# Kernel tuning notes

Measured on AMD Instinct MI355X. Metric: run time of the kernel, lower is better.

The kernel has to match this reference:

```python
import jax, jax.numpy as jnp
import numpy as np

LAYERS, HIDDEN, FFN, HEADS = 4, 128, 256, 4
HEAD_D = HIDDEN // HEADS          # 32
V_HEAD = 2 * HEAD_D               # 64 (double_v_dim)
V_DIM = 2 * HIDDEN                # 256
SCALE_BASE = 512
EPS = 1e-5
GAMMAS = (1.0 - np.exp(np.linspace(np.log(1.0 / 32), np.log(1.0 / 512), HEADS))).astype(np.float32)


def _xpos(x, downscale):
    # x: (..., L, d) -- xpos rotary embedding with per-position decay scale
    L, d = x.shape[-2], x.shape[-1]
    half = d // 2
    base_scale = (jnp.arange(half, dtype=jnp.float32) + 0.4 * d) / (1.4 * d)   # (half,)
    power = jnp.arange(L, dtype=jnp.float32)[:, None] / SCALE_BASE
    sc = base_scale[None, :] ** power                                          # (L, half)
    inv_freq = 1.0 / (10000.0 ** (jnp.arange(half, dtype=jnp.float32) / half))
    ang = jnp.arange(L, dtype=jnp.float32)[:, None] * inv_freq[None, :]        # (L, half)
    sin, cos = jnp.sin(ang), jnp.cos(ang)
    if downscale:
        sc = 1.0 / sc
    sin_d = jnp.repeat(sin * sc, 2, axis=-1)   # duplicate_interleave -> (L, d)
    cos_d = jnp.repeat(cos * sc, 2, axis=-1)
    x1, x2 = x[..., ::2], x[..., 1::2]
    rot = jnp.stack((-x2, x1), axis=-1).reshape(x.shape)  # rotate_every_two
    return x * cos_d + rot * sin_d


def _layer_norm(x, w, b):
    mu = x.mean(-1, keepdims=True)
    var = x.var(-1, keepdims=True)
    return (x - mu) / jnp.sqrt(var + EPS) * w + b


def _msr(X, wq, wk, wv, wg, wo, gn_w, gn_b):
    # MultiScaleRetention, parallel form. X: (B, L, HIDDEN)
    B, L, _ = X.shape
    Q = _xpos(jnp.einsum('blh,nhd->bnld', X, wq), False)   # (B, heads, L, 32)
    K = _xpos(jnp.einsum('blh,nhd->bnld', X, wk), True)
    V = jnp.einsum('blh,nhv->bnlv', X, wv)                 # (B, heads, L, 64)
    n = jnp.arange(L)
    diff = n[:, None] - n[None, :]
    gam = jnp.asarray(GAMMAS)[:, None, None]
    D = jnp.where(diff >= 0, gam ** jnp.maximum(diff, 0).astype(jnp.float32), 0.0)  # (heads, L, L)
    scores = jnp.einsum('bnld,bnmd->bnlm', Q, K) * D[None]
    Y = jnp.einsum('bnlm,bnmv->bnlv', scores, V)
    Y = Y.transpose(0, 2, 1, 3).reshape(B, L, V_DIM)       # concat heads on feature dim
    # GroupNorm(heads, V_DIM) over the channel axis
    Yg = Y.reshape(B, L, HEADS, V_HEAD)
    mu = Yg.mean(-1, keepdims=True)
    var = Yg.var(-1, keepdims=True)
    Yn = ((Yg - mu) / jnp.sqrt(var + EPS)).reshape(B, L, V_DIM) * gn_w + gn_b
    G = X @ wg
    return (G * jax.nn.sigmoid(G) * Yn) @ wo               # swish gate, output proj


def _forward(x, rem_w1, rem_b1, rem_w2, rem_b2, rem_w3, rem_b3,
             wq, wk, wv, wg, wo, gn_w, gn_b,
             ln1_w, ln1_b, ln2_w, ln2_b,
             ffn_w1, ffn_b1, ffn_w2, ffn_b2,
             dec_w1, dec_b1, dec_w2, dec_b2):
    gelu = lambda t: jax.nn.gelu(t, approximate=False)
    # REM: 5 -> 32 -> 64 -> 128, GELU after each linear
    X = gelu(gelu(gelu(x @ rem_w1 + rem_b1) @ rem_w2 + rem_b2) @ rem_w3 + rem_b3)
    # RetNet: pre-LN retention + pre-LN FFN blocks with residuals
    for i in range(LAYERS):
        Y = _msr(_layer_norm(X, ln1_w[i], ln1_b[i]), wq[i], wk[i], wv[i],
                 wg[i], wo[i], gn_w[i], gn_b[i]) + X
        Z = _layer_norm(Y, ln2_w[i], ln2_b[i])
        X = gelu(Z @ ffn_w1[i] + ffn_b1[i]) @ ffn_w2[i] + ffn_b2[i] + Y
    # Decoder: 128 -> 64 -> 20, softmax over classes
    logits = gelu(X @ dec_w1 + dec_b1) @ dec_w2 + dec_b2
    return jax.nn.softmax(logits, axis=-1)


def setup_inputs() -> dict:
    key = jax.random.key(0)
    ks = jax.random.split(key, 16)
    rn = lambda k, shape, s=0.02: jax.random.normal(k, shape, dtype=jnp.float32) * s
    B, L = 64, 512
    return {
        'x': jax.random.normal(ks[0], (B, L, 5), dtype=jnp.float32),
        'rem_w1': rn(ks[1], (5, 32)), 'rem_b1': jnp.zeros((32,), jnp.float32),
        'rem_w2': rn(ks[2], (32, 64)), 'rem_b2': jnp.zeros((64,), jnp.float32),
        'rem_w3': rn(ks[3], (64, HIDDEN)), 'rem_b3': jnp.zeros((HIDDEN,), jnp.float32),
        'wq': rn(ks[4], (LAYERS, HEADS, HIDDEN, HEAD_D), 1.0 / HIDDEN),
        'wk': rn(ks[5], (LAYERS, HEADS, HIDDEN, HEAD_D), 1.0 / HIDDEN),
        'wv': rn(ks[6], (LAYERS, HEADS, HIDDEN, V_HEAD), 1.0 / HIDDEN),
        'wg': rn(ks[7], (LAYERS, HIDDEN, V_DIM), 1.0 / HIDDEN),
        'wo': rn(ks[8], (LAYERS, V_DIM, HIDDEN), 1.0 / HIDDEN),
        'gn_w': jnp.ones((LAYERS, V_DIM), jnp.float32),
        'gn_b': jnp.zeros((LAYERS, V_DIM), jnp.float32),
        'ln1_w': jnp.ones((LAYERS, HIDDEN), jnp.float32),
        'ln1_b': jnp.zeros((LAYERS, HIDDEN), jnp.float32),
        'ln2_w': jnp.ones((LAYERS, HIDDEN), jnp.float32),
        'ln2_b': jnp.zeros((LAYERS, HIDDEN), jnp.float32),
        'ffn_w1': rn(ks[9], (LAYERS, HIDDEN, FFN)),
        'ffn_b1': jnp.zeros((LAYERS, FFN), jnp.float32),
        'ffn_w2': rn(ks[10], (LAYERS, FFN, HIDDEN)),
        'ffn_b2': jnp.zeros((LAYERS, HIDDEN), jnp.float32),
        'dec_w1': rn(ks[11], (HIDDEN, 64)), 'dec_b1': jnp.zeros((64,), jnp.float32),
        'dec_w2': rn(ks[12], (64, 20)), 'dec_b2': jnp.zeros((20,), jnp.float32),
    }


def reference(x, rem_w1, rem_b1, rem_w2, rem_b2, rem_w3, rem_b3,
              wq, wk, wv, wg, wo, gn_w, gn_b,
              ln1_w, ln1_b, ln2_w, ln2_b,
              ffn_w1, ffn_b1, ffn_w2, ffn_b2,
              dec_w1, dec_b1, dec_w2, dec_b2):
    return _forward(x, rem_w1, rem_b1, rem_w2, rem_b2, rem_w3, rem_b3,
                    wq, wk, wv, wg, wo, gn_w, gn_b,
                    ln1_w, ln1_b, ln2_w, ln2_b,
                    ffn_w1, ffn_b1, ffn_w2, ffn_b2,
                    dec_w1, dec_b1, dec_w2, dec_b2)
```

## Files before the change

### kernel.cpp

```cpp
#include <hip/hip_runtime.h>
#include <math.h>
#include <cmath>

#define SEQ   512
#define NBATCH 64
#define BT    32768
#define HID   128
#define NHEAD 4
#define HD    32
#define VHD   64
#define VDIM  256
#define FFND  256

typedef __attribute__((ext_vector_type(8))) short bf16x8;
typedef __attribute__((ext_vector_type(4))) float f32x4;
typedef unsigned short u16;

__device__ __forceinline__ float gelu_f(float x){ return 0.5f*x*(1.f+erff(x*0.70710678118f)); }

__device__ __forceinline__ u16 f2bf(float f){
  union{float f; unsigned u;} v; v.f = f;
  unsigned r = v.u + 0x7FFF + ((v.u>>16)&1);
  return (u16)(r>>16);
}
__device__ __forceinline__ float bf2f(u16 u){
  union{unsigned u; float f;} v; v.u = ((unsigned)u)<<16; return v.f;
}

__device__ __forceinline__ void gload16(const void* g, void* l){
  __builtin_amdgcn_global_load_lds(
      (const __attribute__((address_space(1))) unsigned*)g,
      (__attribute__((address_space(3))) unsigned*)l, 16, 0, 0);
}

#define STAGE_TILE_N(dst, base, strideU16, colOffU16, wid_, srow_, phys16l_, NIT) \
  do{                                                                           \
    _Pragma("unroll")                                                           \
    for(int it_=0; it_<NIT; it_++){                                             \
      int blk_ = (wid_)*NIT + it_;                                              \
      int row_ = blk_*4 + (srow_);                                              \
      int log16_ = (phys16l_) ^ (row_&15);                                      \
      gload16((base) + (size_t)row_*(strideU16) + (colOffU16) + log16_*8,       \
              &(dst)[blk_*512]);                                                \
    }                                                                           \
  }while(0)

#define STAGE_TILE(dst, base, strideU16, colOffU16, wid_, srow_, phys16l_) \
  STAGE_TILE_N(dst, base, strideU16, colOffU16, wid_, srow_, phys16l_, 8)

__global__ __launch_bounds__(256) void wconv_kernel(
    const float* __restrict__ wq, const float* __restrict__ wk,
    const float* __restrict__ wv, const float* __restrict__ wg,
    const float* __restrict__ wo, const float* __restrict__ f1,
    const float* __restrict__ f2, const float* __restrict__ dw1,
    const float* __restrict__ w2e, const float* __restrict__ w3e,
    u16* __restrict__ Wt)
{
  int idx = blockIdx.x*256 + threadIdx.x;
  if(idx >= 786432){
    int q = idx - 786432;
    if(q < 8192){ int col=q>>7, h=q&127; Wt[idx]=f2bf(dw1[h*64+col]); }
    else if(q < 10240){ int p=q-8192; int row=p>>5, col=p&31; Wt[idx]=f2bf(w2e[col*64+row]); }
    else { int p=q-10240; int row=p>>6, col=p&63; Wt[idx]=f2bf(w3e[col*128+row]); }
    return;
  }
  int layer = idx / 196608;
  int r = idx - layer*196608;
  u16* W = Wt + (size_t)layer*196608;
  const float* wq_l = wq + (size_t)layer*16384;
  const float* wk_l = wk + (size_t)layer*16384;
  const float* wv_l = wv + (size_t)layer*32768;
  const float* wg_l = wg + (size_t)layer*32768;
  const float* wo_l = wo + (size_t)layer*32768;
  const float* f1_l = f1 + (size_t)layer*32768;
  const float* f2_l = f2 + (size_t)layer*32768;
  float v;
  if(r < 98304){
    int col = r>>7, h = r&127;
    if(col<128){ int n=col>>5, d=col&31; v = wq_l[(n*128+h)*32+d]; }
    else if(col<256){ int c=col-128, n=c>>5, d=c&31; v = wk_l[(n*128+h)*32+d]; }
    else if(col<512){ int c=col-256, n=c>>6, j=c&63; v = wv_l[(n*128+h)*64+j]; }
    else { int p=col-512; v = wg_l[h*256+p]; }
    W[r] = f2bf(v);
  } else if(r < 131072){
    int q = r-98304; int col=q>>8, k=q&255;
    W[r] = f2bf(wo_l[k*128+col]);
  } else if(r < 163840){
    int q = r-131072; int col=q>>7, h=q&127;
    W[r] = f2bf(f1_l[h*256+col]);
  } else {
    int q = r-163840; int col=q>>8, k=q&255;
    W[r] = f2bf(f2_l[k*128+col]);
  }
}

__global__ __launch_bounds__(256) void embed_kernel(
    const float* __restrict__ x,
    const float* __restrict__ w1, const float* __restrict__ b1,
    const float* __restrict__ b2, const float* __restrict__ b3,
    const u16* __restrict__ W23t,
    const float* __restrict__ lnw, const float* __restrict__ lnb,
    float* __restrict__ X, u16* __restrict__ xn)
{
  __shared__ float sx[64][6];
  __shared__ float sw1[160], sb1[32], sb2[64], sb3[128];
  __shared__ u16 big[18944];
  int t=threadIdx.x, lane=t&63, wid=t>>6, mrow=lane&15, quad=lane>>4, r0=wid*16;
  int tok0=blockIdx.x*64;

  for(int i=t;i<320;i+=256) sx[i/5][i%5]=x[(size_t)tok0*5+i];
  for(int i=t;i<160;i+=256) sw1[i]=w1[i];
  if(t<32) sb1[t]=b1[t];
  if(t<64) sb2[t]=b2[t];
  if(t<128) sb3[t]=b3[t];
  for(int c=t;c<256;c+=256){ int row=c>>2, c8=(c&3)*8;
    *(uint4*)&big[2560+row*40+c8]=*(const uint4*)&W23t[row*32+c8]; }
  for(int c=t;c<1024;c+=256){ int row=c>>3, c8=(c&7)*8;
    *(uint4*)&big[9728+row*72+c8]=*(const uint4*)&W23t[2048+row*64+c8]; }
  __syncthreads();

  for(int task=t; task<2048; task+=256){
    int tok=task>>5, j=task&31;
    float a=sb1[j];
    #pragma unroll
    for(int i=0;i<5;i++) a+=sx[tok][i]*sw1[i*32+j];
    big[tok*40+j]=f2bf(gelu_f(a));
  }
  __syncthreads();

  f32x4 h2[4];
  #pragma unroll
  for(int cc=0;cc<4;cc++) h2[cc]=(f32x4){0.f,0.f,0.f,0.f};
  {
    bf16x8 a=*(const bf16x8*)&big[(r0+mrow)*40+quad*8];
    #pragma unroll
    for(int cc=0;cc<4;cc++){
      bf16x8 b=*(const bf16x8*)&big[2560+(cc*16+mrow)*40+quad*8];
      h2[cc]=__builtin_amdgcn_mfma_f32_16x16x32_bf16(a,b,h2[cc],0,0,0);
    }
  }
  #pragma unroll
  for(int cc=0;cc<4;cc++){
    float bs=sb2[cc*16+mrow];
    #pragma unroll
    for(int reg=0;reg<4;reg++)
      big[5120+(r0+quad*4+reg)*72+cc*16+mrow]=f2bf(gelu_f(h2[cc][reg]+bs));
  }
  __syncthreads();

  f32x4 xac[8];
  #pragma unroll
  for(int cc=0;cc<8;cc++) xac[cc]=(f32x4){0.f,0.f,0.f,0.f};
  #pragma unroll
  for(int ks=0;ks<2;ks++){
    bf16x8 a=*(const bf16x8*)&big[5120+(r0+mrow)*72+ks*32+quad*8];
    #pragma unroll
    for(int cc=0;cc<8;cc++){
      bf16x8 b=*(const bf16x8*)&big[9728+(cc*16+mrow)*72+ks*32+quad*8];
      xac[cc]=__builtin_amdgcn_mfma_f32_16x16x32_bf16(a,b,xac[cc],0,0,0);
    }
  }
  __syncthreads();

  #pragma unroll
  for(int reg=0;reg<4;reg++){
    int rowl=r0+quad*4+reg, rowg=tok0+rowl;
    float xv[8], s=0.f, sq=0.f;
    #pragma unroll
    for(int cc=0;cc<8;cc++){
      float v=gelu_f(xac[cc][reg]+sb3[cc*16+mrow]);
      xv[cc]=v; s+=v; sq+=v*v;
    }
    #pragma unroll
    for(int m=1;m<16;m<<=1){ s+=__shfl_xor(s,m); sq+=__shfl_xor(sq,m); }
    float mu=s*(1.f/128.f);
    float var=sq*(1.f/128.f)-mu*mu;
    float rstd=rsqrtf(var+1e-5f);
    #pragma unroll
    for(int cc=0;cc<8;cc++){
      int col=cc*16+mrow;
      X[(size_t)rowg*128+col]=xv[cc];
      big[rowl*136+col]=f2bf((xv[cc]-mu)*rstd*lnw[col]+lnb[col]);
    }
  }
  __syncthreads();
  for(int th=t; th<1024; th+=256){
    int row=th>>4, seg=th&15;
    *(uint4*)&xn[(size_t)(tok0+row)*128+seg*8]=*(const uint4*)&big[row*136+seg*8];
  }
}

__device__ __forceinline__ void qkvg_epilogue(
    int nc, f32x4 acc[2][4], u16* stg,
    int t, int mrow, int quad, int r0q, int c0q, int b, int l0, int tok0,
    u16* __restrict__ Q, u16* __restrict__ K,
    u16* __restrict__ Vt, u16* __restrict__ G)
{
  if(nc < 2){
    bool isK = (nc==1);
    float sgn = isK ? -1.f : 1.f;
    #pragma unroll
    for(int cc=0;cc<4;cc++){
      int colc = c0q + cc*16 + mrow;
      int i = (colc&31)>>1;
      float log2bs = log2f(((float)i + 12.8f)*(1.f/44.8f));
      float invf   = exp2f(-(float)i * (13.28771238f/16.f));
      float rstep  = exp2f(sgn*log2bs*(1.f/512.f));
      float c1 = cosf(invf), s1 = sinf(invf);
      #pragma unroll
      for(int rr=0;rr<2;rr++){
        int rowl0 = r0q + rr*16 + quad*4;
        float lb = (float)(l0 + rowl0);
        float sc = exp2f(sgn*log2bs*lb*(1.f/512.f));
        float ang = lb*invf;
        float u = cosf(ang)*sc, v = sinf(ang)*sc;
        #pragma unroll
        for(int reg=0;reg<4;reg++){
          int rowl = rowl0 + reg;
          float val = acc[rr][cc][reg];
          float partner = __shfl_xor(val, 1);
          float o = (colc&1) ? (val*u + partner*v) : (val*u - partner*v);
          stg[rowl*136 + colc] = f2bf(o);
          float un = (u*c1 - v*s1)*rstep;
          float vn = (u*s1 + v*c1)*rstep;
          u = un; v = vn;
        }
      }
    }
    __syncthreads();
    u16* O = isK ? K : Q;
    for(int th=t; th<1024; th+=256){
      int row=th>>4, n=(th>>2)&3, seg=th&3;
      *(uint4*)&O[(((size_t)(b*4+n)*512) + (l0+row))*32 + seg*8]
        = *(const uint4*)&stg[row*136 + n*32 + seg*8];
    }
  } else if(nc < 4){
    #pragma unroll
    for(int cc=0;cc<4;cc++){
      int colc = c0q + cc*16 + mrow;
      #pragma unroll
      for(int rr=0;rr<2;rr++){
        #pragma unroll
        for(int reg=0;reg<4;reg++){
          int rowl = r0q + rr*16 + quad*4 + reg;
          stg[colc*72 + rowl] = f2bf(acc[rr][cc][reg]);
        }
      }
    }
    __syncthreads();
    int jbase = (nc-2)*128;
    for(int th=t; th<1024; th+=256){
      int row=th>>3, seg=th&7;
      int jg = jbase + row; int n = jg>>6, j = jg&63;
      *(uint4*)&Vt[(((size_t)(b*4+n)*64) + j)*512 + l0 + seg*8]
        = *(const uint4*)&stg[row*72 + seg*8];
    }
  } else {
    #pragma unroll
    for(int cc=0;cc<4;cc++){
      int colc = c0q + cc*16 + mrow;
      #pragma unroll
      for(int rr=0;rr<2;rr++){
        #pragma unroll
        for(int reg=0;reg<4;reg++){
          int rowl = r0q + rr*16 + quad*4 + reg;
          stg[rowl*136 + colc] = f2bf(acc[rr][cc][reg]);
        }
      }
    }
    __syncthreads();
    int gc0 = (nc-4)*128;
    for(int th=t; th<1024; th+=256){
      int row=th>>4, seg=th&15;
      *(uint4*)&G[((size_t)(tok0+row))*256 + gc0 + seg*8]
        = *(const uint4*)&stg[row*136 + seg*8];
    }
  }
}

__device__ __forceinline__ void qkvg_epi8(
    int nc, f32x4 acc[4], u16* stg,
    int t, int mrow, int quad, int r0, int c0, int b, int l0, int tok0,
    u16* __restrict__ Q, u16* __restrict__ K,
    u16* __restrict__ Vt, u16* __restrict__ G)
{
  if(nc < 2){
    bool isK = (nc==1);
    float sgn = isK ? -1.f : 1.f;
    #pragma unroll
    for(int cc=0;cc<4;cc++){
      int colc = c0 + cc*16 + mrow;
      int i = (colc&31)>>1;
      float log2bs = log2f(((float)i + 12.8f)*(1.f/44.8f));
      float invf   = exp2f(-(float)i * (13.28771238f/16.f));
      float rstep  = exp2f(sgn*log2bs*(1.f/512.f));
      float c1 = cosf(invf), s1 = sinf(invf);
      int rowl0 = r0 + quad*4;
      float lb = (float)(l0 + rowl0);
      float sc = exp2f(sgn*log2bs*lb*(1.f/512.f));
      float ang = lb*invf;
      float u = cosf(ang)*sc, v = sinf(ang)*sc;
      #pragma unroll
      for(int reg=0;reg<4;reg++){
        int rowl = rowl0 + reg;
        float val = acc[cc][reg];
        float partner = __shfl_xor(val, 1);
        float o = (colc&1) ? (val*u + partner*v) : (val*u - partner*v);
        stg[rowl*136 + colc] = f2bf(o);
        float un = (u*c1 - v*s1)*rstep;
        float vn = (u*s1 + v*c1)*rstep;
        u = un; v = vn;
      }
    }
    __syncthreads();
    u16* O = isK ? K : Q;
    for(int th=t; th<1024; th+=512){
      int row=th>>4, n=(th>>2)&3, seg=th&3;
      *(uint4*)&O[(((size_t)(b*4+n)*512) + (l0+row))*32 + seg*8]
        = *(const uint4*)&stg[row*136 + n*32 + seg*8];
    }
  } else if(nc < 4){
    #pragma unroll
    for(int cc=0;cc<4;cc++){
      int colc = c0 + cc*16 + mrow;
      #pragma unroll
      for(int reg=0;reg<4;reg++){
        int rowl = r0 + quad*4 + reg;
        stg[colc*72 + rowl] = f2bf(acc[cc][reg]);
      }
    }
    __syncthreads();
    int jbase = (nc-2)*128;
    for(int th=t; th<1024; th+=512){
      int row=th>>3, seg=th&7;
      int jg = jbase + row; int n = jg>>6, j = jg&63;
      *(uint4*)&Vt[(((size_t)(b*4+n)*64) + j)*512 + l0 + seg*8]
        = *(const uint4*)&stg[row*72 + seg*8];
    }
  } else {
    #pragma unroll
    for(int cc=0;cc<4;cc++){
      int colc = c0 + cc*16 + mrow;
      #pragma unroll
      for(int reg=0;reg<4;reg++){
        int rowl = r0 + quad*4 + reg;
        stg[rowl*136 + colc] = f2bf(acc[cc][reg]);
      }
    }
    __syncthreads();
    int gc0 = (nc-4)*128;
    for(int th=t; th<1024; th+=512){
      int row=th>>4, seg=th&15;
      *(uint4*)&G[((size_t)(tok0+row))*256 + gc0 + seg*8]
        = *(const uint4*)&stg[row*136 + seg*8];
    }
  }
}

__global__ __launch_bounds__(256) void qkvg_kernel(
    const u16* __restrict__ A, const u16* __restrict__ Wt,
    u16* __restrict__ Q, u16* __restrict__ K,
    u16* __restrict__ Vt, u16* __restrict__ G)
{
  __shared__ u16 sW[128*128];
  u16* stg = sW;
  int t = threadIdx.x, lane = t&63, wid = t>>6;
  int mrow = lane&15, quad = lane>>4;
  int srow = lane>>4, phys16l = lane&15;
  int r0q = (wid>>1)*32, c0q = (wid&1)*64;
  int tok0 = blockIdx.x*64;
  int b = tok0>>9, l0 = tok0&511;

  bf16x8 a0f[4], a1f[4];
  #pragma unroll
  for(int ks=0; ks<4; ks++){
    a0f[ks] = *(const bf16x8*)&A[(size_t)(tok0+r0q+mrow)*128 + ks*32+quad*8];
    a1f[ks] = *(const bf16x8*)&A[(size_t)(tok0+r0q+16+mrow)*128 + ks*32+quad*8];
  }

  for(int ch=0; ch<3; ch++){
    int nc = blockIdx.y*3 + ch;
    if(ch) __syncthreads();
    STAGE_TILE(sW, Wt + (size_t)nc*16384, 128, 0, wid, srow, phys16l);
    __syncthreads();

    f32x4 acc[2][4];
    #pragma unroll
    for(int rr=0;rr<2;rr++)
      #pragma unroll
      for(int cc=0;cc<4;cc++) acc[rr][cc] = (f32x4){0.f,0.f,0.f,0.f};
    #pragma unroll
    for(int ks=0; ks<4; ks++){
      #pragma unroll
      for(int cc=0; cc<4; cc++){
        bf16x8 bb = *(const bf16x8*)&sW[(c0q+cc*16+mrow)*128 + (((ks*4+quad)^mrow)<<3)];
        acc[0][cc] = __builtin_amdgcn_mfma_f32_16x16x32_bf16(a0f[ks],bb,acc[0][cc],0,0,0);
        acc[1][cc] = __builtin_amdgcn_mfma_f32_16x16x32_bf16(a1f[ks],bb,acc[1][cc],0,0,0);
      }
    }
    __syncthreads();
    qkvg_epilogue(nc, acc, stg, t, mrow, quad, r0q, c0q, b, l0, tok0, Q, K, Vt, G);
  }
}

__global__ __launch_bounds__(512, 4) void mlpq_kernel(
    const u16* __restrict__ Gated, const u16* __restrict__ Wo,
    const u16* __restrict__ W1t, const float* __restrict__ b1,
    const u16* __restrict__ W2t, const float* __restrict__ b2,
    const float* __restrict__ Xin,
    const float* __restrict__ ln2w, const float* __restrict__ ln2b,
    const float* __restrict__ ln1w, const float* __restrict__ ln1b,
    float* __restrict__ Xout,
    const u16* __restrict__ Wq,
    u16* __restrict__ Q, u16* __restrict__ K,
    u16* __restrict__ Vt, u16* __restrict__ G)
{
  __shared__ u16 sW[128*128];
  __shared__ u16 sT[64*136];
  __shared__ float sRed[64][2][2];
  int t=threadIdx.x, lane=t&63, wid=t>>6, mrow=lane&15, quad=lane>>4;
  int rg=wid>>1, half=wid&1;
  int r0=rg*16, c0=half*64;
  int tok0=blockIdx.x*64;
  int srow = lane>>4, phys16l = lane&15;

  bf16x8 gfrag[8];
  #pragma unroll
  for(int ks=0;ks<8;ks++)
    gfrag[ks]=*(const bf16x8*)&Gated[(size_t)(tok0+r0+mrow)*256 + ks*32+quad*8];

  f32x4 yac[4];
  #pragma unroll
  for(int cc=0;cc<4;cc++) yac[cc]=(f32x4){0.f,0.f,0.f,0.f};
  STAGE_TILE_N(sW, Wo, 256, 0, wid, srow, phys16l, 4);
  __syncthreads();
  #pragma unroll
  for(int kh=0; kh<2; kh++){
    #pragma unroll
    for(int cc=0;cc<4;cc++){
      #pragma unroll
      for(int ks=0;ks<4;ks++){
        bf16x8 b=*(const bf16x8*)&sW[(c0+cc*16+mrow)*128 + (((ks*4+quad)^mrow)<<3)];
        yac[cc]=__builtin_amdgcn_mfma_f32_16x16x32_bf16(gfrag[kh*4+ks],b,yac[cc],0,0,0);
      }
    }
    if(kh==0){
      __syncthreads();
      STAGE_TILE_N(sW, Wo, 256, 128, wid, srow, phys16l, 4);
      __syncthreads();
    }
  }

  float yv[4][4];
  #pragma unroll
  for(int reg=0;reg<4;reg++){
    int rowl=r0+quad*4+reg, rowg=tok0+rowl;
    float s=0.f, sq=0.f;
    #pragma unroll
    for(int cc=0;cc<4;cc++){
      float v=yac[cc][reg]+Xin[(size_t)rowg*128+c0+cc*16+mrow];
      yv[cc][reg]=v; s+=v; sq+=v*v;
    }
    #pragma unroll
    for(int m=1;m<16;m<<=1){ s+=__shfl_xor(s,m); sq+=__shfl_xor(sq,m); }
    if(mrow==0){ sRed[rowl][half][0]=s; sRed[rowl][half][1]=sq; }
  }
  __syncthreads();
  #pragma unroll
  for(int reg=0;reg<4;reg++){
    int rowl=r0+quad*4+reg;
    float s =sRed[rowl][0][0]+sRed[rowl][1][0];
    float sq=sRed[rowl][0][1]+sRed[rowl][1][1];
    float mu=s*(1.f/128.f);
    float var=sq*(1.f/128.f)-mu*mu;
    float rstd=rsqrtf(var+1e-5f);
    #pragma unroll
    for(int cc=0;cc<4;cc++){
      int col=c0+cc*16+mrow;
      sT[rowl*136+col]=f2bf((yv[cc][reg]-mu)*rstd*ln2w[col]+ln2b[col]);
    }
  }
  __syncthreads();
  bf16x8 az[4];
  #pragma unroll
  for(int ks=0;ks<4;ks++) az[ks]=*(const bf16x8*)&sT[(r0+mrow)*136+ks*32+quad*8];

  bf16x8 hfrag[8];
  #pragma unroll
  for(int nh=0; nh<2; nh++){
    STAGE_TILE_N(sW, W1t + (size_t)nh*16384, 128, 0, wid, srow, phys16l, 4);
    __syncthreads();
    f32x4 hac[4];
    #pragma unroll
    for(int cc=0;cc<4;cc++) hac[cc]=(f32x4){0.f,0.f,0.f,0.f};
    #pragma unroll
    for(int cc=0;cc<4;cc++){
      #pragma unroll
      for(int ks=0;ks<4;ks++){
        bf16x8 b=*(const bf16x8*)&sW[(c0+cc*16+mrow)*128 + (((ks*4+quad)^mrow)<<3)];
        hac[cc]=__builtin_amdgcn_mfma_f32_16x16x32_bf16(az[ks],b,hac[cc],0,0,0);
      }
    }
    __syncthreads();
    #pragma unroll
    for(int cc=0;cc<4;cc++){
      float bs=b1[nh*128+c0+cc*16+mrow];
      #pragma unroll
      for(int reg=0;reg<4;reg++)
        sT[(r0+quad*4+reg)*136 + c0+cc*16+mrow]=f2bf(gelu_f(hac[cc][reg]+bs));
    }
    __syncthreads();
    #pragma unroll
    for(int ks=0;ks<4;ks++) hfrag[nh*4+ks]=*(const bf16x8*)&sT[(r0+mrow)*136+ks*32+quad*8];
  }

  f32x4 xac[4];
  #pragma unroll
  for(int cc=0;cc<4;cc++) xac[cc]=(f32x4){0.f,0.f,0.f,0.f};
  STAGE_TILE_N(sW, W2t, 256, 0, wid, srow, phys16l, 4);
  __syncthreads();
  #pragma unroll
  for(int kh=0; kh<2; kh++){
    #pragma unroll
    for(int cc=0;cc<4;cc++){
      #pragma unroll
      for(int ks=0;ks<4;ks++){
        bf16x8 b=*(const bf16x8*)&sW[(c0+cc*16+mrow)*128 + (((ks*4+quad)^mrow)<<3)];
        xac[cc]=__builtin_amdgcn_mfma_f32_16x16x32_bf16(hfrag[kh*4+ks],b,xac[cc],0,0,0);
      }
    }
    __syncthreads();
    if(kh==0){
      STAGE_TILE_N(sW, W2t, 256, 128, wid, srow, phys16l, 4);
      __syncthreads();
    }
  }

  float* fst = (float*)sW;
  float xv[4][4];
  #pragma unroll
  for(int reg=0;reg<4;reg++){
    int rowl=r0+quad*4+reg;
    float s=0.f, sq=0.f;
    #pragma unroll
    for(int cc=0;cc<4;cc++){
      float v=xac[cc][reg]+b2[c0+cc*16+mrow]+yv[cc][reg];
      xv[cc][reg]=v; s+=v; sq+=v*v;
    }
    #pragma unroll
    for(int m=1;m<16;m<<=1){ s+=__shfl_xor(s,m); sq+=__shfl_xor(sq,m); }
    if(mrow==0){ sRed[rowl][half][0]=s; sRed[rowl][half][1]=sq; }
  }
  __syncthreads();
  #pragma unroll
  for(int reg=0;reg<4;reg++){
    int rowl=r0+quad*4+reg;
    float s =sRed[rowl][0][0]+sRed[rowl][1][0];
    float sq=sRed[rowl][0][1]+sRed[rowl][1][1];
    float mu=s*(1.f/128.f);
    float var=sq*(1.f/128.f)-mu*mu;
    float rstd=rsqrtf(var+1e-5f);
    #pragma unroll
    for(int cc=0;cc<4;cc++){
      int col=c0+cc*16+mrow;
      fst[rowl*128+col]=xv[cc][reg];
      sT[rowl*136+col]=f2bf((xv[cc][reg]-mu)*rstd*ln1w[col]+ln1b[col]);
    }
  }
  __syncthreads();
  for(int th=t; th<2048; th+=512){
    int row=th>>5, c4=(th&31)*4;
    *(float4*)&Xout[(size_t)(tok0+row)*128+c4]=*(const float4*)&fst[row*128+c4];
  }

  if(!Wq) return;

  int b = tok0>>9, l0 = tok0&511;
  bf16x8 aq[4];
  #pragma unroll
  for(int ks=0; ks<4; ks++)
    aq[ks] = *(const bf16x8*)&sT[(r0+mrow)*136 + ks*32+quad*8];
  __syncthreads();

  for(int nc=0; nc<6; nc++){
    if(nc) __syncthreads();
    STAGE_TILE_N(sW, Wq + (size_t)nc*16384, 128, 0, wid, srow, phys16l, 4);
    __syncthreads();

    f32x4 acc[4];
    #pragma unroll
    for(int cc=0;cc<4;cc++) acc[cc] = (f32x4){0.f,0.f,0.f,0.f};
    #pragma unroll
    for(int ks=0; ks<4; ks++){
      #pragma unroll
      for(int cc=0; cc<4; cc++){
        bf16x8 bb = *(const bf16x8*)&sW[(c0+cc*16+mrow)*128 + (((ks*4+quad)^mrow)<<3)];
        acc[cc] = __builtin_amdgcn_mfma_f32_16x16x32_bf16(aq[ks],bb,acc[cc],0,0,0);
      }
    }
    __syncthreads();
    qkvg_epi8(nc, acc, sW, t, mrow, quad, r0, c0, b, l0, tok0, Q, K, Vt, G);
  }
}

__global__ __launch_bounds__(256) void retmfma_kernel(
    const u16* __restrict__ Q, const u16* __restrict__ K,
    const u16* __restrict__ Vt, const u16* __restrict__ G,
    const float* __restrict__ gnw, const float* __restrict__ gnb,
    u16* __restrict__ Gated, float4 log2g)
{
  int idx = blockIdx.x;
  int bn = ((idx>>6)<<3) | (idx&7);
  int lt = (idx>>3)&7;
  int n = bn & 3, b = bn >> 2;
  float lg2g = (n==0)?log2g.x:(n==1)?log2g.y:(n==2)?log2g.z:log2g.w;
  __shared__ u16 sK[64][40];
  __shared__ u16 sVt[64][72];
  __shared__ u16 sS[64][72];
  int t = threadIdx.x, lane = t&63, wid = t>>6;
  int mrow = lane&15, quad = lane>>4;
  int r0 = wid*16;

  bf16x8 qa = *(const bf16x8*)&Q[((size_t)bn*512 + lt*64 + r0+mrow)*32 + quad*8];

  f32x4 oacc[4];
  #pragma unroll
  for(int cc=0;cc<4;cc++) oacc[cc] = (f32x4){0.f,0.f,0.f,0.f};
  float gp1 = exp2f(lg2g), gp2 = gp1*gp1, gp3 = gp2*gp1;
  float gpow[4] = {1.f, gp1, gp2, gp3};
  float gw[4], gb[4];
  #pragma unroll
  for(int cc=0;cc<4;cc++){ gw[cc]=gnw[n*64+cc*16+mrow]; gb[cc]=gnb[n*64+cc*16+mrow]; }
  int rowl0 = lt*64 + r0 + quad*4;

  for(int mt=0; mt<=lt; mt++){
    if(mt) __syncthreads();
    {
      int row = t>>2, c8 = (t&3)*8;
      *(uint4*)&sK[row][c8] = *(const uint4*)&K[((size_t)bn*512 + mt*64 + row)*32 + c8];
      int vrow = t>>3, vc8 = (t&7)*8;
      *(uint4*)&sVt[vrow][vc8]    = *(const uint4*)&Vt[((size_t)bn*64 + vrow)*512    + mt*64 + vc8];
      *(uint4*)&sVt[vrow+32][vc8] = *(const uint4*)&Vt[((size_t)bn*64 + vrow+32)*512 + mt*64 + vc8];
    }
    __syncthreads();
    f32x4 sacc[4];
    #pragma unroll
    for(int cc=0;cc<4;cc++){
      bf16x8 bb = *(const bf16x8*)&sK[cc*16+mrow][quad*8];
      sacc[cc] = __builtin_amdgcn_mfma_f32_16x16x32_bf16(qa,bb,(f32x4){0.f,0.f,0.f,0.f},0,0,0);
    }
    #pragma unroll
    for(int cc=0;cc<4;cc++){
      int colm = mt*64 + cc*16 + mrow;
      int d0 = rowl0 - colm;
      float w0 = exp2f(lg2g*(float)d0);
      #pragma unroll
      for(int reg=0;reg<4;reg++){
        float w = (d0+reg>=0) ? w0*gpow[reg] : 0.f;
        sS[r0+quad*4+reg][cc*16+mrow] = f2bf(sacc[cc][reg]*w);
      }
    }
    __syncthreads();
    #pragma unroll
    for(int ks=0;ks<2;ks++){
      bf16x8 a = *(const bf16x8*)&sS[r0+mrow][ks*32+quad*8];
      #pragma unroll
      for(int cc=0;cc<4;cc++){
        bf16x8 bb = *(const bf16x8*)&sVt[cc*16+mrow][ks*32+quad*8];
        oacc[cc] = __builtin_amdgcn_mfma_f32_16x16x32_bf16(a,bb,oacc[cc],0,0,0);
      }
    }
  }

  __syncthreads();
  #pragma unroll
  for(int reg=0;reg<4;reg++){
    float s=0.f, sq=0.f;
    #pragma unroll
    for(int cc=0;cc<4;cc++){ float v=oacc[cc][reg]; s+=v; sq+=v*v; }
    #pragma unroll
    for(int m=1;m<16;m<<=1){ s+=__shfl_xor(s,m); sq+=__shfl_xor(sq,m); }
    float mu = s*(1.f/64.f);
    float var = sq*(1.f/64.f) - mu*mu;
    float rn = rsqrtf(var + 1e-5f);
    int rowl = r0 + quad*4 + reg;
    int l = lt*64 + rowl;
    size_t gbase = ((size_t)(b*512 + l))*256 + n*64;
    #pragma unroll
    for(int cc=0;cc<4;cc++){
      float gg = bf2f(G[gbase + cc*16+mrow]);
      float gate = gg/(1.f+expf(-gg));
      sS[rowl][cc*16+mrow] = f2bf(gate*((oacc[cc][reg]-mu)*rn*gw[cc] + gb[cc]));
    }
  }
  __syncthreads();
  for(int th=t; th<512; th+=256){
    int row=th>>3, seg=th&7;
    *(uint4*)&Gated[((size_t)(b*512 + lt*64 + row))*256 + n*64 + seg*8]
      = *(const uint4*)&sS[row][seg*8];
  }
}

__global__ __launch_bounds__(256) void dec_kernel(
    const float* __restrict__ X, const u16* __restrict__ W1t,
    const float* __restrict__ b1, const float* __restrict__ w2,
    const float* __restrict__ b2, float* __restrict__ out)
{
  __shared__ u16 sA[64][136];
  __shared__ u16 sW[64][136];
  __shared__ float sH[64][68];
  __shared__ float sL[64*20];
  __shared__ float sw2[64*20];
  __shared__ float sb2[20];
  int t = threadIdx.x, lane = t&63, wid = t>>6;
  int mrow = lane&15, quad = lane>>4;
  int tok0 = blockIdx.x*64;

  for(int th=t; th<2048; th+=256){
    int row=th>>5, c4=(th&31)*4;
    float4 v = *(const float4*)&X[(size_t)(tok0+row)*128 + c4];
    ushort4 p; p.x=f2bf(v.x); p.y=f2bf(v.y); p.z=f2bf(v.z); p.w=f2bf(v.w);
    *(ushort4*)&sA[row][c4] = p;
  }
  for(int th=t; th<1024; th+=256){
    int row=th>>4, c8=(th&15)*8;
    *(uint4*)&sW[row][c8] = *(const uint4*)&W1t[(size_t)row*128 + c8];
  }
  for(int i=t;i<1280;i+=256) sw2[i]=w2[i];
  if(t<20) sb2[t]=b2[t];
  __syncthreads();

  int r0 = wid*16;
  f32x4 acc[4];
  #pragma unroll
  for(int cc=0;cc<4;cc++) acc[cc] = (f32x4){0.f,0.f,0.f,0.f};
  #pragma unroll
  for(int ks=0; ks<4; ks++){
    int koff = ks*32 + quad*8;
    bf16x8 a = *(const bf16x8*)&sA[r0+mrow][koff];
    #pragma unroll
    for(int cc=0; cc<4; cc++){
      bf16x8 b = *(const bf16x8*)&sW[cc*16+mrow][koff];
      acc[cc] = __builtin_amdgcn_mfma_f32_16x16x32_bf16(a,b,acc[cc],0,0,0);
    }
  }
  #pragma unroll
  for(int cc=0;cc<4;cc++){
    int col = cc*16 + mrow;
    float bb = b1[col];
    #pragma unroll
    for(int reg=0;reg<4;reg++){
      sH[r0 + quad*4 + reg][col] = gelu_f(acc[cc][reg] + bb);
    }
  }
  __syncthreads();

  for(int task=t; task<1280; task+=256){
    int tk = task/20, o = task - tk*20;
    float a = sb2[o];
    for(int k=0;k<64;k++) a += sH[tk][k]*sw2[k*20+o];
    sL[tk*20+o] = a;
  }
  __syncthreads();
  if(t < 64){
    float mx = -1e30f;
    #pragma unroll
    for(int o=0;o<20;o++) mx = fmaxf(mx, sL[t*20+o]);
    float sum = 0.f;
    float e[20];
    #pragma unroll
    for(int o=0;o<20;o++){ e[o]=expf(sL[t*20+o]-mx); sum += e[o]; }
    float inv = 1.f/sum;
    #pragma unroll
    for(int o=0;o<20;o++) sL[t*20+o] = e[o]*inv;
  }
  __syncthreads();
  for(int th=t; th<1280; th+=256){
    out[(size_t)tok0*20 + th] = sL[th];
  }
}

extern "C" void kernel_launch(void* const* d_in, const int* in_sizes, int n_in,
                              void* d_out, int out_size, void* d_ws, size_t ws_size,
                              hipStream_t stream) {
  (void)in_sizes; (void)n_in; (void)out_size; (void)ws_size;
  const float* x      = (const float*)d_in[0];
  const float* rem_w1 = (const float*)d_in[1];
  const float* rem_b1 = (const float*)d_in[2];
  const float* rem_w2 = (const float*)d_in[3];
  const float* rem_b2 = (const float*)d_in[4];
  const float* rem_w3 = (const float*)d_in[5];
  const float* rem_b3 = (const float*)d_in[6];
  const float* wq     = (const float*)d_in[7];
  const float* wk     = (const float*)d_in[8];
  const float* wv     = (const float*)d_in[9];
  const float* wg     = (const float*)d_in[10];
  const float* wo     = (const float*)d_in[11];
  const float* gn_w   = (const float*)d_in[12];
  const float* gn_b   = (const float*)d_in[13];
  const float* ln1_w  = (const float*)d_in[14];
  const float* ln1_b  = (const float*)d_in[15];
  const float* ln2_w  = (const float*)d_in[16];
  const float* ln2_b  = (const float*)d_in[17];
  const float* ffn_w1 = (const float*)d_in[18];
  const float* ffn_b1 = (const float*)d_in[19];
  const float* ffn_w2 = (const float*)d_in[20];
  const float* ffn_b2 = (const float*)d_in[21];
  const float* dec_w1 = (const float*)d_in[22];
  const float* dec_b1 = (const float*)d_in[23];
  const float* dec_w2 = (const float*)d_in[24];
  const float* dec_b2 = (const float*)d_in[25];
  float* outp = (float*)d_out;

  const size_t S128 = (size_t)BT*128;
  const size_t S256 = (size_t)BT*256;
  float* ws = (float*)d_ws;
  float* Xb = ws;
  u16*  Qb16    = (u16*)(Xb + S128);
  u16*  Kb16    = Qb16 + (size_t)BT*32;
  u16*  Vt16    = Kb16 + (size_t)BT*32;
  u16*  XnBf    = Vt16 + (size_t)BT*64;
  u16*  GBf     = XnBf + S128;
  u16*  GatedBf = GBf + S256;
  u16*  WtBf    = GatedBf + S256;

  double lgA = log(1.0/32.0), lgB = log(1.0/512.0);
  float4 l2g;
  {
    double g0 = 1.0 - exp(lgA + 0.0*(lgB-lgA)/3.0);
    double g1 = 1.0 - exp(lgA + 1.0*(lgB-lgA)/3.0);
    double g2 = 1.0 - exp(lgA + 2.0*(lgB-lgA)/3.0);
    double g3 = 1.0 - exp(lgA + 3.0*(lgB-lgA)/3.0);
    l2g.x = (float)(log(g0)/log(2.0));
    l2g.y = (float)(log(g1)/log(2.0));
    l2g.z = (float)(log(g2)/log(2.0));
    l2g.w = (float)(log(g3)/log(2.0));
  }

  wconv_kernel<<<3144, 256, 0, stream>>>(wq, wk, wv, wg, wo, ffn_w1, ffn_w2, dec_w1,
                                         rem_w2, rem_w3, WtBf);
  embed_kernel<<<BT/64, 256, 0, stream>>>(x, rem_w1, rem_b1, rem_b2, rem_b3,
                                          WtBf+794624, ln1_w, ln1_b, Xb, XnBf);
  qkvg_kernel<<<dim3(BT/64,2), 256, 0, stream>>>(XnBf, WtBf, Qb16, Kb16, Vt16, GBf);

  for(int li=0; li<4; li++){
    u16* Wt_l = WtBf + (size_t)li*196608;
    const float* gnw_l = gn_w + (size_t)li*VDIM;
    const float* gnb_l = gn_b + (size_t)li*VDIM;
    const float* l2w = ln2_w + (size_t)li*HID, *l2b = ln2_b + (size_t)li*HID;
    const float* f1b = ffn_b1 + (size_t)li*FFND;
    const float* f2b = ffn_b2 + (size_t)li*HID;
    int nli = (li+1)&3;
    const float* n1w = ln1_w + (size_t)nli*HID, *n1b = ln1_b + (size_t)nli*HID;
    const u16* Wq_next = (li<3) ? (WtBf + (size_t)(li+1)*196608) : nullptr;

    retmfma_kernel<<<2048, 256, 0, stream>>>(Qb16, Kb16, Vt16, GBf, gnw_l, gnb_l, GatedBf, l2g);
    mlpq_kernel<<<BT/64, 512, 0, stream>>>(
        GatedBf, Wt_l+98304, Wt_l+131072, f1b, Wt_l+163840, f2b,
        Xb, l2w, l2b, n1w, n1b, Xb,
        Wq_next, Qb16, Kb16, Vt16, GBf);
  }

  dec_kernel<<<BT/64, 256, 0, stream>>>(Xb, WtBf+786432, dec_b1, dec_w2, dec_b2, outp);
}
```

Measured before the change: 454.7 us.

## Prefetch next weight tile into registers while computing current tile in fused FFN kernel

Replaces the direct global-to-LDS weight staging with a register double-buffer. The next weight tile is loaded into registers while the MFMAs on the current LDS tile run, then written to LDS at the next stage. Xin is also loaded early into registers. The aim is to hide global load latency behind compute, at the cost of extra VGPRs and explicit LDS stores.

```diff
diff --git a/kernel.cpp b/kernel.cpp
--- a/kernel.cpp
+++ b/kernel.cpp
@@ -47,6 +47,26 @@
 
 #define STAGE_TILE(dst, base, strideU16, colOffU16, wid_, srow_, phys16l_) \
   STAGE_TILE_N(dst, base, strideU16, colOffU16, wid_, srow_, phys16l_, 8)
+
+#define PREF_TILE(regs, base, strideU16, colOffU16, wid_, srow_, phys16l_, NIT)  \
+  do{                                                                           \
+    _Pragma("unroll")                                                           \
+    for(int it_=0; it_<NIT; it_++){                                             \
+      int blk_ = (wid_)*NIT + it_;                                              \
+      int row_ = blk_*4 + (srow_);                                              \
+      int log16_ = (phys16l_) ^ (row_&15);                                      \
+      (regs)[it_] = *(const uint4*)((base) + (size_t)row_*(strideU16) + (colOffU16) + log16_*8); \
+    }                                                                           \
+  }while(0)
+
+#define WRITE_TILE(dst, regs, wid_, lane_, NIT)                                 \
+  do{                                                                           \
+    _Pragma("unroll")                                                           \
+    for(int it_=0; it_<NIT; it_++){                                             \
+      int blk_ = (wid_)*NIT + it_;                                              \
+      *(uint4*)&(dst)[blk_*512 + (lane_)*8] = (regs)[it_];                      \
+    }                                                                           \
+  }while(0)
 
 __global__ __launch_bounds__(256) void wconv_kernel(
     const float* __restrict__ wq, const float* __restrict__ wk,
@@ -424,41 +444,57 @@
   int tok0=blockIdx.x*64;
   int srow = lane>>4, phys16l = lane&15;
 
+  uint4 pf[4];
+  PREF_TILE(pf, Wo, 256, 0, wid, srow, phys16l, 4);
+
   bf16x8 gfrag[8];
   #pragma unroll
   for(int ks=0;ks<8;ks++)
     gfrag[ks]=*(const bf16x8*)&Gated[(size_t)(tok0+r0+mrow)*256 + ks*32+quad*8];
+  float xinv[4][4];
+  #pragma unroll
+  for(int reg=0;reg<4;reg++){
+    #pragma unroll
+    for(int cc=0;cc<4;cc++)
+      xinv[cc][reg]=Xin[(size_t)(tok0+r0+quad*4+reg)*128 + c0+cc*16+mrow];
+  }
+
+  WRITE_TILE(sW, pf, wid, lane, 4);
+  PREF_TILE(pf, Wo, 256, 128, wid, srow, phys16l, 4);
+  __syncthreads();
 
   f32x4 yac[4];
   #pragma unroll
   for(int cc=0;cc<4;cc++) yac[cc]=(f32x4){0.f,0.f,0.f,0.f};
-  STAGE_TILE_N(sW, Wo, 256, 0, wid, srow, phys16l, 4);
-  __syncthreads();
-  #pragma unroll
-  for(int kh=0; kh<2; kh++){
-    #pragma unroll
-    for(int cc=0;cc<4;cc++){
-      #pragma unroll
-      for(int ks=0;ks<4;ks++){
-        bf16x8 b=*(const bf16x8*)&sW[(c0+cc*16+mrow)*128 + (((ks*4+quad)^mrow)<<3)];
-        yac[cc]=__builtin_amdgcn_mfma_f32_16x16x32_bf16(gfrag[kh*4+ks],b,yac[cc],0,0,0);
-      }
-    }
-    if(kh==0){
-      __syncthreads();
-      STAGE_TILE_N(sW, Wo, 256, 128, wid, srow, phys16l, 4);
-      __syncthreads();
+  #pragma unroll
+  for(int cc=0;cc<4;cc++){
+    #pragma unroll
+    for(int ks=0;ks<4;ks++){
+      bf16x8 b=*(const bf16x8*)&sW[(c0+cc*16+mrow)*128 + (((ks*4+quad)^mrow)<<3)];
+      yac[cc]=__builtin_amdgcn_mfma_f32_16x16x32_bf16(gfrag[ks],b,yac[cc],0,0,0);
+    }
+  }
+  __syncthreads();
+  WRITE_TILE(sW, pf, wid, lane, 4);
+  PREF_TILE(pf, W1t, 128, 0, wid, srow, phys16l, 4);
+  __syncthreads();
+  #pragma unroll
+  for(int cc=0;cc<4;cc++){
+    #pragma unroll
+    for(int ks=0;ks<4;ks++){
+      bf16x8 b=*(const bf16x8*)&sW[(c0+cc*16+mrow)*128 + (((ks*4+quad)^mrow)<<3)];
+      yac[cc]=__builtin_amdgcn_mfma_f32_16x16x32_bf16(gfrag[4+ks],b,yac[cc],0,0,0);
     }
   }
 
   float yv[4][4];
   #pragma unroll
   for(int reg=0;reg<4;reg++){
-    int rowl=r0+quad*4+reg, rowg=tok0+rowl;
+    int rowl=r0+quad*4+reg;
     float s=0.f, sq=0.f;
     #pragma unroll
     for(int cc=0;cc<4;cc++){
-      float v=yac[cc][reg]+Xin[(size_t)rowg*128+c0+cc*16+mrow];
+      float v=yac[cc][reg]+xinv[cc][reg];
       yv[cc][reg]=v; s+=v; sq+=v*v;
     }
     #pragma unroll
@@ -488,7 +524,9 @@
   bf16x8 hfrag[8];
   #pragma unroll
   for(int nh=0; nh<2; nh++){
-    STAGE_TILE_N(sW, W1t + (size_t)nh*16384, 128, 0, wid, srow, phys16l, 4);
+    WRITE_TILE(sW, pf, wid, lane, 4);
+    if(nh==0) PREF_TILE(pf, W1t + (size_t)16384, 128, 0, wid, srow, phys16l, 4);
+    else      PREF_TILE(pf, W2t, 256, 0, wid, srow, phys16l, 4);
     __syncthreads();
     f32x4 hac[4];
     #pragma unroll
@@ -517,24 +555,30 @@
   f32x4 xac[4];
   #pragma unroll
   for(int cc=0;cc<4;cc++) xac[cc]=(f32x4){0.f,0.f,0.f,0.f};
-  STAGE_TILE_N(sW, W2t, 256, 0, wid, srow, phys16l, 4);
-  __syncthreads();
-  #pragma unroll
-  for(int kh=0; kh<2; kh++){
-    #pragma unroll
-    for(int cc=0;cc<4;cc++){
-      #pragma unroll
-      for(int ks=0;ks<4;ks++){
-        bf16x8 b=*(const bf16x8*)&sW[(c0+cc*16+mrow)*128 + (((ks*4+quad)^mrow)<<3)];
-        xac[cc]=__builtin_amdgcn_mfma_f32_16x16x32_bf16(hfrag[kh*4+ks],b,xac[cc],0,0,0);
-      }
-    }
-    __syncthreads();
-    if(kh==0){
-      STAGE_TILE_N(sW, W2t, 256, 128, wid, srow, phys16l, 4);
-      __syncthreads();
-    }
-  }
+  WRITE_TILE(sW, pf, wid, lane, 4);
+  PREF_TILE(pf, W2t, 256, 128, wid, srow, phys16l, 4);
+  __syncthreads();
+  #pragma unroll
+  for(int cc=0;cc<4;cc++){
+    #pragma unroll
+    for(int ks=0;ks<4;ks++){
+      bf16x8 b=*(const bf16x8*)&sW[(c0+cc*16+mrow)*128 + (((ks*4+quad)^mrow)<<3)];
+      xac[cc]=__builtin_amdgcn_mfma_f32_16x16x32_bf16(hfrag[ks],b,xac[cc],0,0,0);
+    }
+  }
+  __syncthreads();
+  WRITE_TILE(sW, pf, wid, lane, 4);
+  if(Wq) PREF_TILE(pf, Wq, 128, 0, wid, srow, phys16l, 4);
+  __syncthreads();
+  #pragma unroll
+  for(int cc=0;cc<4;cc++){
+    #pragma unroll
+    for(int ks=0;ks<4;ks++){
+      bf16x8 b=*(const bf16x8*)&sW[(c0+cc*16+mrow)*128 + (((ks*4+quad)^mrow)<<3)];
+      xac[cc]=__builtin_amdgcn_mfma_f32_16x16x32_bf16(hfrag[4+ks],b,xac[cc],0,0,0);
+    }
+  }
+  __syncthreads();
 
   float* fst = (float*)sW;
   float xv[4][4];
@@ -584,7 +628,8 @@
 
   for(int nc=0; nc<6; nc++){
     if(nc) __syncthreads();
-    STAGE_TILE_N(sW, Wq + (size_t)nc*16384, 128, 0, wid, srow, phys16l, 4);
+    WRITE_TILE(sW, pf, wid, lane, 4);
+    if(nc<5) PREF_TILE(pf, Wq + (size_t)(nc+1)*16384, 128, 0, wid, srow, phys16l, 4);
     __syncthreads();
 
     f32x4 acc[4];
```

New measurement: 558.7 us. 22.9% more time.

## Double-buffer weight tiles in the fused MLP/QKV kernel to overlap staging with MFMA

Applied to the files above, without the earlier changes.

Shared memory is rearranged into two 16K-element weight buffers. The next weight tile (Wo second half, W1t halves, W2t halves, Wq chunks) is staged into one buffer while MFMAs read the other, which removes the serialized load-then-compute barriers. The fp32 staging of Xout through shared memory is replaced by direct per-element global stores. The trade-off is a larger static LDS footprint (about 65KB versus about 50KB per block), which may reduce resident blocks per CU. The Xout stores are also less coalesced.

```diff
diff --git a/kernel.cpp b/kernel.cpp
--- a/kernel.cpp
+++ b/kernel.cpp
@@ -415,42 +415,46 @@
     u16* __restrict__ Q, u16* __restrict__ K,
     u16* __restrict__ Vt, u16* __restrict__ G)
 {
-  __shared__ u16 sW[128*128];
-  __shared__ u16 sT[64*136];
+  __shared__ u16 sW[32768];
   __shared__ float sRed[64][2][2];
+  u16* bufA = sW;
+  u16* bufB = sW + 16384;
   int t=threadIdx.x, lane=t&63, wid=t>>6, mrow=lane&15, quad=lane>>4;
   int rg=wid>>1, half=wid&1;
   int r0=rg*16, c0=half*64;
   int tok0=blockIdx.x*64;
   int srow = lane>>4, phys16l = lane&15;
 
+  STAGE_TILE_N(bufA, Wo, 256, 0, wid, srow, phys16l, 4);
   bf16x8 gfrag[8];
   #pragma unroll
   for(int ks=0;ks<8;ks++)
     gfrag[ks]=*(const bf16x8*)&Gated[(size_t)(tok0+r0+mrow)*256 + ks*32+quad*8];
-
+  __syncthreads();
+
+  STAGE_TILE_N(bufB, Wo, 256, 128, wid, srow, phys16l, 4);
   f32x4 yac[4];
   #pragma unroll
   for(int cc=0;cc<4;cc++) yac[cc]=(f32x4){0.f,0.f,0.f,0.f};
-  STAGE_TILE_N(sW, Wo, 256, 0, wid, srow, phys16l, 4);
-  __syncthreads();
-  #pragma unroll
-  for(int kh=0; kh<2; kh++){
-    #pragma unroll
-    for(int cc=0;cc<4;cc++){
-      #pragma unroll
-      for(int ks=0;ks<4;ks++){
-        bf16x8 b=*(const bf16x8*)&sW[(c0+cc*16+mrow)*128 + (((ks*4+quad)^mrow)<<3)];
-        yac[cc]=__builtin_amdgcn_mfma_f32_16x16x32_bf16(gfrag[kh*4+ks],b,yac[cc],0,0,0);
-      }
-    }
-    if(kh==0){
-      __syncthreads();
-      STAGE_TILE_N(sW, Wo, 256, 128, wid, srow, phys16l, 4);
-      __syncthreads();
-    }
-  }
-
+  #pragma unroll
+  for(int cc=0;cc<4;cc++){
+    #pragma unroll
+    for(int ks=0;ks<4;ks++){
+      bf16x8 b=*(const bf16x8*)&bufA[(c0+cc*16+mrow)*128 + (((ks*4+quad)^mrow)<<3)];
+      yac[cc]=__builtin_amdgcn_mfma_f32_16x16x32_bf16(gfrag[ks],b,yac[cc],0,0,0);
+    }
+  }
+  __syncthreads();
+
+  STAGE_TILE_N(bufA, W1t, 128, 0, wid, srow, phys16l, 4);
+  #pragma unroll
+  for(int cc=0;cc<4;cc++){
+    #pragma unroll
+    for(int ks=0;ks<4;ks++){
+      bf16x8 b=*(const bf16x8*)&bufB[(c0+cc*16+mrow)*128 + (((ks*4+quad)^mrow)<<3)];
+      yac[cc]=__builtin_amdgcn_mfma_f32_16x16x32_bf16(gfrag[4+ks],b,yac[cc],0,0,0);
+    }
+  }
   float yv[4][4];
   #pragma unroll
   for(int reg=0;reg<4;reg++){
@@ -466,6 +470,7 @@
     if(mrow==0){ sRed[rowl][half][0]=s; sRed[rowl][half][1]=sq; }
   }
   __syncthreads();
+
   #pragma unroll
   for(int reg=0;reg<4;reg++){
     int rowl=r0+quad*4+reg;
@@ -477,19 +482,18 @@
     #pragma unroll
     for(int cc=0;cc<4;cc++){
       int col=c0+cc*16+mrow;
-      sT[rowl*136+col]=f2bf((yv[cc][reg]-mu)*rstd*ln2w[col]+ln2b[col]);
+      bufB[rowl*136+col]=f2bf((yv[cc][reg]-mu)*rstd*ln2w[col]+ln2b[col]);
     }
   }
   __syncthreads();
   bf16x8 az[4];
   #pragma unroll
-  for(int ks=0;ks<4;ks++) az[ks]=*(const bf16x8*)&sT[(r0+mrow)*136+ks*32+quad*8];
+  for(int ks=0;ks<4;ks++) az[ks]=*(const bf16x8*)&bufB[(r0+mrow)*136+ks*32+quad*8];
+  __syncthreads();
 
   bf16x8 hfrag[8];
-  #pragma unroll
-  for(int nh=0; nh<2; nh++){
-    STAGE_TILE_N(sW, W1t + (size_t)nh*16384, 128, 0, wid, srow, phys16l, 4);
-    __syncthreads();
+  STAGE_TILE_N(bufB, W1t + (size_t)16384, 128, 0, wid, srow, phys16l, 4);
+  {
     f32x4 hac[4];
     #pragma unroll
     for(int cc=0;cc<4;cc++) hac[cc]=(f32x4){0.f,0.f,0.f,0.f};
@@ -497,46 +501,74 @@
     for(int cc=0;cc<4;cc++){
       #pragma unroll
       for(int ks=0;ks<4;ks++){
-        bf16x8 b=*(const bf16x8*)&sW[(c0+cc*16+mrow)*128 + (((ks*4+quad)^mrow)<<3)];
+        bf16x8 b=*(const bf16x8*)&bufA[(c0+cc*16+mrow)*128 + (((ks*4+quad)^mrow)<<3)];
         hac[cc]=__builtin_amdgcn_mfma_f32_16x16x32_bf16(az[ks],b,hac[cc],0,0,0);
       }
     }
     __syncthreads();
     #pragma unroll
     for(int cc=0;cc<4;cc++){
-      float bs=b1[nh*128+c0+cc*16+mrow];
+      float bs=b1[c0+cc*16+mrow];
       #pragma unroll
       for(int reg=0;reg<4;reg++)
-        sT[(r0+quad*4+reg)*136 + c0+cc*16+mrow]=f2bf(gelu_f(hac[cc][reg]+bs));
-    }
-    __syncthreads();
-    #pragma unroll
-    for(int ks=0;ks<4;ks++) hfrag[nh*4+ks]=*(const bf16x8*)&sT[(r0+mrow)*136+ks*32+quad*8];
-  }
-
+        bufA[(r0+quad*4+reg)*136 + c0+cc*16+mrow]=f2bf(gelu_f(hac[cc][reg]+bs));
+    }
+    __syncthreads();
+    #pragma unroll
+    for(int ks=0;ks<4;ks++) hfrag[ks]=*(const bf16x8*)&bufA[(r0+mrow)*136+ks*32+quad*8];
+    __syncthreads();
+  }
+
+  STAGE_TILE_N(bufA, W2t, 256, 0, wid, srow, phys16l, 4);
+  {
+    f32x4 hac[4];
+    #pragma unroll
+    for(int cc=0;cc<4;cc++) hac[cc]=(f32x4){0.f,0.f,0.f,0.f};
+    #pragma unroll
+    for(int cc=0;cc<4;cc++){
+      #pragma unroll
+      for(int ks=0;ks<4;ks++){
+        bf16x8 b=*(const bf16x8*)&bufB[(c0+cc*16+mrow)*128 + (((ks*4+quad)^mrow)<<3)];
+        hac[cc]=__builtin_amdgcn_mfma_f32_16x16x32_bf16(az[ks],b,hac[cc],0,0,0);
+      }
+    }
+    __syncthreads();
+    #pragma unroll
+    for(int cc=0;cc<4;cc++){
+      float bs=b1[128+c0+cc*16+mrow];
+      #pragma unroll
+      for(int reg=0;reg<4;reg++)
+        bufB[(r0+quad*4+reg)*136 + c0+cc*16+mrow]=f2bf(gelu_f(hac[cc][reg]+bs));
+    }
+    __syncthreads();
+    #pragma unroll
+    for(int ks=0;ks<4;ks++) hfrag[4+ks]=*(const bf16x8*)&bufB[(r0+mrow)*136+ks*32+quad*8];
+    __syncthreads();
+  }
+
+  STAGE_TILE_N(bufB, W2t, 256, 128, wid, srow, phys16l, 4);
   f32x4 xac[4];
   #pragma unroll
   for(int cc=0;cc<4;cc++) xac[cc]=(f32x4){0.f,0.f,0.f,0.f};
-  STAGE_TILE_N(sW, W2t, 256, 0, wid, srow, phys16l, 4);
-  __syncthreads();
-  #pragma unroll
-  for(int kh=0; kh<2; kh++){
-    #pragma unroll
-    for(int cc=0;cc<4;cc++){
-      #pragma unroll
-      for(int ks=0;ks<4;ks++){
-        bf16x8 b=*(const bf16x8*)&sW[(c0+cc*16+mrow)*128 + (((ks*4+quad)^mrow)<<3)];
-        xac[cc]=__builtin_amdgcn_mfma_f32_16x16x32_bf16(hfrag[kh*4+ks],b,xac[cc],0,0,0);
-      }
-    }
-    __syncthreads();
-    if(kh==0){
-      STAGE_TILE_N(sW, W2t, 256, 128, wid, srow, phys16l, 4);
-      __syncthreads();
-    }
-  }
-
-  float* fst = (float*)sW;
+  #pragma unroll
+  for(int cc=0;cc<4;cc++){
+    #pragma unroll
+    for(int ks=0;ks<4;ks++){
+      bf16x8 b=*(const bf16x8*)&bufA[(c0+cc*16+mrow)*128 + (((ks*4+quad)^mrow)<<3)];
+      xac[cc]=__builtin_amdgcn_mfma_f32_16x16x32_bf16(hfrag[ks],b,xac[cc],0,0,0);
+    }
+  }
+  __syncthreads();
+
+  if(Wq) STAGE_TILE_N(bufA, Wq, 128, 0, wid, srow, phys16l, 4);
+  #pragma unroll
+  for(int cc=0;cc<4;cc++){
+    #pragma unroll
+    for(int ks=0;ks<4;ks++){
+      bf16x8 b=*(const bf16x8*)&bufB[(c0+cc*16+mrow)*128 + (((ks*4+quad)^mrow)<<3)];
+      xac[cc]=__builtin_amdgcn_mfma_f32_16x16x32_bf16(hfrag[4+ks],b,xac[cc],0,0,0);
+    }
+  }
   float xv[4][4];
   #pragma unroll
   for(int reg=0;reg<4;reg++){
@@ -552,9 +584,10 @@
     if(mrow==0){ sRed[rowl][half][0]=s; sRed[rowl][half][1]=sq; }
   }
   __syncthreads();
+
   #pragma unroll
   for(int reg=0;reg<4;reg++){
-    int rowl=r0+quad*4+reg;
+    int rowl=r0+quad*4+reg, rowg=tok0+rowl;
     float s =sRed[rowl][0][0]+sRed[rowl][1][0];
     float sq=sRed[rowl][0][1]+sRed[rowl][1][1];
     float mu=s*(1.f/128.f);
@@ -563,29 +596,23 @@
     #pragma unroll
     for(int cc=0;cc<4;cc++){
       int col=c0+cc*16+mrow;
-      fst[rowl*128+col]=xv[cc][reg];
-      sT[rowl*136+col]=f2bf((xv[cc][reg]-mu)*rstd*ln1w[col]+ln1b[col]);
-    }
-  }
-  __syncthreads();
-  for(int th=t; th<2048; th+=512){
-    int row=th>>5, c4=(th&31)*4;
-    *(float4*)&Xout[(size_t)(tok0+row)*128+c4]=*(const float4*)&fst[row*128+c4];
-  }
-
+      Xout[(size_t)rowg*128+col]=xv[cc][reg];
+      if(Wq) bufB[rowl*136+col]=f2bf((xv[cc][reg]-mu)*rstd*ln1w[col]+ln1b[col]);
+    }
+  }
   if(!Wq) return;
+  __syncthreads();
+  bf16x8 aq[4];
+  #pragma unroll
+  for(int ks=0; ks<4; ks++)
+    aq[ks] = *(const bf16x8*)&bufB[(r0+mrow)*136 + ks*32+quad*8];
+  __syncthreads();
 
   int b = tok0>>9, l0 = tok0&511;
-  bf16x8 aq[4];
-  #pragma unroll
-  for(int ks=0; ks<4; ks++)
-    aq[ks] = *(const bf16x8*)&sT[(r0+mrow)*136 + ks*32+quad*8];
-  __syncthreads();
-
   for(int nc=0; nc<6; nc++){
-    if(nc) __syncthreads();
-    STAGE_TILE_N(sW, Wq + (size_t)nc*16384, 128, 0, wid, srow, phys16l, 4);
-    __syncthreads();
+    u16* cur = (nc&1) ? bufB : bufA;
+    u16* nxt = (nc&1) ? bufA : bufB;
+    if(nc<5) STAGE_TILE_N(nxt, Wq + (size_t)(nc+1)*16384, 128, 0, wid, srow, phys16l, 4);
 
     f32x4 acc[4];
     #pragma unroll
@@ -594,12 +621,13 @@
     for(int ks=0; ks<4; ks++){
       #pragma unroll
       for(int cc=0; cc<4; cc++){
-        bf16x8 bb = *(const bf16x8*)&sW[(c0+cc*16+mrow)*128 + (((ks*4+quad)^mrow)<<3)];
+        bf16x8 bb = *(const bf16x8*)&cur[(c0+cc*16+mrow)*128 + (((ks*4+quad)^mrow)<<3)];
         acc[cc] = __builtin_amdgcn_mfma_f32_16x16x32_bf16(aq[ks],bb,acc[cc],0,0,0);
       }
     }
     __syncthreads();
-    qkvg_epi8(nc, acc, sW, t, mrow, quad, r0, c0, b, l0, tok0, Q, K, Vt, G);
+    qkvg_epi8(nc, acc, cur, t, mrow, quad, r0, c0, b, l0, tok0, Q, K, Vt, G);
+    __syncthreads();
   }
 }
 
```

Result: no change. 451.3 us (-0.7%).
